# Kernel tuning notes

Measured on AMD Instinct MI355X. Metric: run time of the kernel, lower is better.

Reference implementation:

```python
import jax, jax.numpy as jnp
import numpy as np

NA, NC = 5, 20          # num_anchors, num_classes
EPS, SLOPE = 1e-5, 0.1  # BatchNorm eps, LeakyReLU slope


def _conv(x, w, pad):
    return jax.lax.conv_general_dilated(
        x, w, (1, 1), [(pad, pad), (pad, pad)],
        dimension_numbers=("NCHW", "OIHW", "NCHW"))


def _cbl(x, w, g, b, m, v, pad):
    # Conv2dBatchLeaky: conv (no bias) + eval-mode BN + LeakyReLU(0.1)
    x = _conv(x, w, pad)
    scale = (g * jax.lax.rsqrt(v + EPS))[None, :, None, None]
    shift = (b - m * g * jax.lax.rsqrt(v + EPS))[None, :, None, None]
    x = x * scale + shift
    return jnp.where(x > 0, x, SLOPE * x)


def _reorg(x, s=2):
    # faithful lightnet Reorg: out channels = s*s*C, spatial halved
    B, C, H, W = x.shape
    x = x.reshape(B, C, H // s, s, W // s, s)
    x = x.transpose(0, 1, 2, 4, 3, 5)                 # B,C,H/s,W/s,s,s
    x = x.reshape(B, C, (H // s) * (W // s), s * s)
    x = x.transpose(0, 1, 3, 2)                        # B,C,s*s,HW/s^2
    x = x.reshape(B, C, s * s, H // s, W // s)
    x = x.transpose(0, 2, 1, 3, 4)                     # B,s*s,C,H/s,W/s
    return x.reshape(B, s * s * C, H // s, W // s)


def setup_inputs() -> dict:
    key = jax.random.key(0)
    ks = jax.random.split(key, 16)
    B = 16
    return {
        "feat0": jax.random.normal(ks[0], (B, 1024, 19, 19), jnp.float32),
        "feat1": jax.random.normal(ks[1], (B, 512, 38, 38), jnp.float32),
        "w1": jax.random.normal(ks[2], (64, 512, 1, 1), jnp.float32) * 0.05,
        "g1": jax.random.uniform(ks[3], (64,), jnp.float32, 0.5, 1.5),
        "b1": jax.random.normal(ks[4], (64,), jnp.float32) * 0.05,
        "m1": jax.random.normal(ks[5], (64,), jnp.float32) * 0.05,
        "v1": jax.random.uniform(ks[6], (64,), jnp.float32, 0.5, 1.5),
        "w2": jax.random.normal(ks[7], (1024, 1280, 3, 3), jnp.float32) * 0.01,
        "g2": jax.random.uniform(ks[8], (1024,), jnp.float32, 0.5, 1.5),
        "b2": jax.random.normal(ks[9], (1024,), jnp.float32) * 0.05,
        "m2": jax.random.normal(ks[10], (1024,), jnp.float32) * 0.05,
        "v2": jax.random.uniform(ks[11], (1024,), jnp.float32, 0.5, 1.5),
        "wd": jax.random.normal(ks[12], (30, 1024, 1, 1), jnp.float32) * 0.02,
        "bd": jax.random.normal(ks[13], (30,), jnp.float32) * 0.02,
    }


def reference(feat0, feat1, w1, g1, b1, m1, v1, w2, g2, b2, m2, v2, wd, bd):
    stage6_reorg = _reorg(_cbl(feat1, w1, g1, b1, m1, v1, pad=0))   # B,256,19,19
    pre = _cbl(jnp.concatenate([stage6_reorg, feat0], axis=1),
               w2, g2, b2, m2, v2, pad=1)                            # B,1024,19,19
    B, C, H, W = pre.shape
    # one-hot reweighting mask: channel c belongs to class (c mod NC)
    rew = (jnp.mod(jnp.arange(C, dtype=jnp.float32), NC)[None, :]
           == jnp.arange(NC, dtype=jnp.float32)[:, None]).astype(pre.dtype)  # NC,C
    tiled = pre[:, None] * rew[None, :, :, None, None]               # B,NC,C,H,W
    pred = _conv(tiled.reshape(B * NC, C, H, W), wd, pad=0) \
        + bd[None, :, None, None]                                    # B*NC,30,H,W
    gp = pred.reshape(B, NC, NA, 6, H, W).transpose(0, 2, 1, 3, 4, 5)  # B,NA,NC,6,H,W
    cls = gp[:, :, :, 5]                                             # B,NA,NC,H,W
    ids = jnp.argmax(cls, axis=2)                                    # B,NA,H,W
    g05 = jnp.take_along_axis(gp[:, :, :, :5],
                              ids[:, :, None, None], axis=2)[:, :, 0]  # B,NA,5,H,W
    final = jnp.concatenate([g05, cls], axis=2)                      # B,NA,25,H,W
    return final.reshape(B, NA * (5 + NC), H, W)
```

## Files before the change

### kernel.cpp

```cpp
#include <hip/hip_runtime.h>
#include <hip/hip_bf16.h>

#define EPSV 1e-5f
#define SLOPEV 0.1f
#define AS1 __attribute__((address_space(1)))
#define AS3 __attribute__((address_space(3)))

typedef __attribute__((ext_vector_type(8))) _Float16 h8;
typedef __attribute__((ext_vector_type(4))) float f32x4;
typedef unsigned int uint32;
typedef unsigned short ushort_t;

#define PLANE       ((size_t)18063360)
#define WSPLIT_OFF  ((size_t)36126720)
#define PRE_OFF     ((size_t)124968960)

#define APREC  28224
#define BB     56448
#define BBUF   24576
#define SMEMSZ 105600

__device__ __forceinline__ void split2_pack(const float* f, uint32* ph, uint32* pm) {
#pragma unroll
  for (int i = 0; i < 4; ++i) {
    float a = f[2 * i], b = f[2 * i + 1];
    _Float16 ha = (_Float16)a, hb = (_Float16)b;
    float ra = (a - (float)ha) * 2048.f;
    float rb = (b - (float)hb) * 2048.f;
    _Float16 ma = (_Float16)ra, mb = (_Float16)rb;
    ph[i] = (uint32)__builtin_bit_cast(ushort_t, ha) | ((uint32)__builtin_bit_cast(ushort_t, hb) << 16);
    pm[i] = (uint32)__builtin_bit_cast(ushort_t, ma) | ((uint32)__builtin_bit_cast(ushort_t, mb) << 16);
  }
}

__global__ __launch_bounds__(256) void k_prep(
    const float* __restrict__ feat1, const float* __restrict__ w1,
    const float* __restrict__ g1, const float* __restrict__ b1,
    const float* __restrict__ m1, const float* __restrict__ v1,
    const float* __restrict__ feat0, const float* __restrict__ w2,
    char* __restrict__ nbase, char* __restrict__ wsp)
{
  __shared__ __attribute__((aligned(16))) float S[8192];
  const int bid = blockIdx.x;
  const int t = threadIdx.x;

  if (bid < 384) {
    const int bx = bid % 6, cq = (bid / 6) % 4, b = bid / 24;
#pragma unroll
    for (int i = 0; i < 8; ++i) {
      int f4 = t + i * 256;
      int j = f4 >> 7, c4 = (f4 & 127) * 4;
      *(float4*)&S[j * 512 + c4] = *(const float4*)&w1[(cq * 16 + j) * 512 + c4];
    }
    __syncthreads();
    const int p = bx * 256 + t;
    const int pp = p < 1444 ? p : 1443;
    const float* xp = feat1 + (size_t)(b * 512) * 1444 + pp;
    float acc[16];
#pragma unroll
    for (int j = 0; j < 16; ++j) acc[j] = 0.f;
#pragma unroll 2
    for (int c4 = 0; c4 < 512; c4 += 4) {
      float x0 = xp[(size_t)(c4 + 0) * 1444];
      float x1 = xp[(size_t)(c4 + 1) * 1444];
      float x2 = xp[(size_t)(c4 + 2) * 1444];
      float x3 = xp[(size_t)(c4 + 3) * 1444];
#pragma unroll
      for (int j = 0; j < 16; ++j) {
        float4 w = *(const float4*)&S[j * 512 + c4];
        acc[j] = fmaf(x0, w.x, acc[j]);
        acc[j] = fmaf(x1, w.y, acc[j]);
        acc[j] = fmaf(x2, w.z, acc[j]);
        acc[j] = fmaf(x3, w.w, acc[j]);
      }
    }
    if (p >= 1444) return;
#pragma unroll
    for (int j = 0; j < 16; ++j) {
      int co = cq * 16 + j;
      float sc = g1[co] / sqrtf(v1[co] + EPSV);
      float sh = b1[co] - m1[co] * sc;
      float v = fmaf(acc[j], sc, sh);
      acc[j] = v > 0.f ? v : SLOPEV * v;
    }
    int y = p / 38, x = p - (p / 38) * 38;
    int q = ((y & 1) << 1) | (x & 1);
    int s = (1 + (y >> 1)) * 21 + 1 + (x >> 1);
    const int sw = (s >> 1) & 3;
    size_t rowb = ((size_t)(b * 441 + s)) * 2560;
    int grp = (q * 64 + cq * 16) >> 5;
    char* d0 = nbase + rowb + grp * 64;
#pragma unroll
    for (int u = 0; u < 2; ++u) {
      int q4 = ((cq & 1) << 1) | u;
      uint32 H[4], M[4];
      split2_pack(&acc[u * 8], H, M);
      int off = (q4 ^ sw) << 4;
      *(uint4*)(d0 + off)         = make_uint4(H[0], H[1], H[2], H[3]);
      *(uint4*)(d0 + PLANE + off) = make_uint4(M[0], M[1], M[2], M[3]);
    }

  } else if (bid < 1984) {
    int gid = (bid - 384) * 256 + t;
    int c16 = gid % 160;
    int r = gid / 160;
    int bp = r % 80;
    int pi = r / 80;
    int s;
    if (bp < 21) s = bp;
    else if (bp < 42) s = 399 + bp;
    else if (bp < 61) s = (bp - 41) * 21;
    else s = (bp - 60) * 21 + 20;
    int plane = pi >> 4, img = pi & 15;
    *(uint4*)(nbase + (size_t)plane * PLANE + ((size_t)(img * 441 + s)) * 2560 + c16 * 16)
        = make_uint4(0u, 0u, 0u, 0u);

  } else if (bid < 4544) {
    const int blk = bid - 1984;
    const int cc = blk >> 6, nt = (blk >> 2) & 15, nj = blk & 3;
    const float* src = w2 + ((size_t)(nt * 64 + nj * 16) * 1280 + cc * 32) * 9;
#pragma unroll
    for (int i = 0; i < 18; ++i) {
      int idx = t + i * 256;
      int col = idx / 288, d = idx - col * 288;
      S[col * 289 + d] = src[(size_t)col * 11520 + d];
    }
    __syncthreads();
#pragma unroll
    for (int it = 0; it < 3; ++it) {
      int u = t + it * 256;
      if (u < 576) {
        int tap = u / 64, kq = (u >> 4) & 3, ln = u & 15;
        float f[8];
#pragma unroll
        for (int c8 = 0; c8 < 8; ++c8) f[c8] = S[ln * 289 + (kq * 8 + c8) * 9 + tap] * 32.f;
        uint32 H[4], M[4];
        split2_pack(f, H, M);
        size_t ob = ((size_t)(cc * 16 + nt) * 9 + tap) * 8192 + nj * 1024
                  + (kq * 16 + ln) * 16;
        *(uint4*)(wsp + ob)        = make_uint4(H[0], H[1], H[2], H[3]);
        *(uint4*)(wsp + ob + 4096) = make_uint4(M[0], M[1], M[2], M[3]);
      }
    }

  } else {
    const int bid4 = bid - 4544;
    const int px = bid4 % 6, cy = (bid4 / 6) % 16, b = bid4 / 96;
    const int p0 = px * 64, c0 = 256 + cy * 64;
#pragma unroll
    for (int j = 0; j < 16; ++j) {
      int c_l = (t >> 6) + j * 4;
      int p_l = t & 63;
      float v = 0.f;
      int pos = p0 + p_l;
      if (pos < 361)
        v = feat0[((size_t)(b * 1024 + (c0 - 256) + c_l)) * 361 + pos];
      S[c_l * 65 + p_l] = v;
    }
    __syncthreads();
#pragma unroll
    for (int jj = 0; jj < 2; ++jj) {
      int p_l = (t >> 3) + jj * 32;
      int cgrp = t & 7;
      int pos = p0 + p_l;
      if (pos < 361) {
        int y = pos / 19, x = pos - (pos / 19) * 19;
        int s = (y + 1) * 21 + x + 1;
        float f[8];
#pragma unroll
        for (int u = 0; u < 8; ++u) f[u] = S[(cgrp * 8 + u) * 65 + p_l];
        uint32 H[4], M[4];
        split2_pack(f, H, M);
        int ch8 = c0 + cgrp * 8;
        int grp = ch8 >> 5, q4 = (ch8 >> 3) & 3;
        size_t byteo = ((size_t)(b * 441 + s)) * 2560 + grp * 64
                     + ((q4 ^ ((s >> 1) & 3)) << 4);
        *(uint4*)(nbase + byteo)         = make_uint4(H[0], H[1], H[2], H[3]);
        *(uint4*)(nbase + PLANE + byteo) = make_uint4(M[0], M[1], M[2], M[3]);
      }
    }
  }
}

#define A_ADDR(IDX_) (nbase + (size_t)((IDX_) / 1764) * PLANE + imgbase \
                      + (size_t)((((IDX_) - ((IDX_) / 1764) * 1764)) >> 2) * 2560 \
                      + (ccn << 1) + ((((IDX_) - ((IDX_) / 1764) * 1764) & 3) << 4))

__global__ __launch_bounds__(512, 2) void k_conv2(
    const char* __restrict__ nbase, const char* __restrict__ wsp,
    const float* __restrict__ g2, const float* __restrict__ b2,
    const float* __restrict__ m2, const float* __restrict__ v2,
    float* __restrict__ pre)
{
  __shared__ __attribute__((aligned(16))) unsigned char smem[SMEMSZ];

  const int bid = blockIdx.x;
  const int ntile = (bid & 7) + 8 * ((bid >> 3) & 1);
  const int img = bid >> 4;
  const int co0 = ntile * 64;

  const int tid = threadIdx.x;
  const int wv = tid >> 6;
  const int lane = tid & 63;
  const int ln = lane & 15;
  const int q = lane >> 4;

  int arow[3];
#pragma unroll
  for (int mi = 0; mi < 3; ++mi) {
    int p = wv * 48 + mi * 16 + ln;
    p = p > 360 ? 360 : p;
    arow[mi] = (p / 19) * 21 + (p - (p / 19) * 19);
  }

  f32x4 acc0[3][4], acc1[3][4];
#pragma unroll
  for (int mi = 0; mi < 3; ++mi)
#pragma unroll
    for (int nj = 0; nj < 4; ++nj) { acc0[mi][nj] = (f32x4)0.f; acc1[mi][nj] = (f32x4)0.f; }

  const size_t imgbase = (size_t)(img * 441) * 2560;
  const size_t wnt = (size_t)ntile * 9 * 8192;

#pragma unroll
  for (int i = 0; i < 7; ++i) {
    int idx = tid + i * 512;
    if (idx < 3528) {
      int pr = idx / 1764;
      int r  = idx - pr * 1764;
      const char* src = nbase + (size_t)pr * PLANE + imgbase
                      + (size_t)(r >> 2) * 2560 + ((r & 3) << 4);
      __builtin_amdgcn_global_load_lds((const AS1 uint32*)src,
          (AS3 uint32*)(smem + idx * 16), 16, 0, 0);
    }
  }
  {
    const char* bs = wsp + wnt;
#pragma unroll
    for (int i = 0; i < 3; ++i) {
      int idx = tid + i * 512;
      __builtin_amdgcn_global_load_lds((const AS1 uint32*)(bs + idx * 16),
          (AS3 uint32*)(smem + BB + idx * 16), 16, 0, 0);
    }
  }

  uint4 ar0, ar1, ar2, ar3, ar4, ar5, ar6;

#pragma unroll 1
  for (int cc = 0; cc < 1280; cc += 32) {
    __syncthreads();

    const int ccn = cc + 32;
    const bool pn = ccn < 1280;
    if (pn) {
      ar0 = *(const uint4*)A_ADDR(tid + 0 * 512);
      ar1 = *(const uint4*)A_ADDR(tid + 1 * 512);
      ar2 = *(const uint4*)A_ADDR(tid + 2 * 512);
      ar3 = *(const uint4*)A_ADDR(tid + 3 * 512);
      ar4 = *(const uint4*)A_ADDR(tid + 4 * 512);
      ar5 = *(const uint4*)A_ADDR(tid + 5 * 512);
      if (tid < 456) {
        int r = tid + 3072 - 1764;
        ar6 = *(const uint4*)(nbase + PLANE + imgbase
                + (size_t)(r >> 2) * 2560 + (ccn << 1) + ((r & 3) << 4));
      }
    }

#pragma unroll
    for (int p = 0; p < 3; ++p) {
      const int P = (cc >> 5) * 3 + p;
      if (P + 1 < 120) {
        const int nc = (P + 1) / 3, ntb = ((P + 1) - nc * 3) * 3;
        const char* bs = wsp + ((size_t)nc * 144 + (size_t)ntb) * 8192 + wnt;
        char* bd = (char*)smem + BB + ((P + 1) & 1) * BBUF;
#pragma unroll
        for (int i = 0; i < 3; ++i) {
          int idx = tid + i * 512;
          __builtin_amdgcn_global_load_lds((const AS1 uint32*)(bs + idx * 16),
              (AS3 uint32*)(bd + idx * 16), 16, 0, 0);
        }
      }

      const unsigned char* bufR = smem + BB + (P & 1) * BBUF;
      __builtin_amdgcn_s_setprio(1);
#pragma unroll
      for (int t3 = 0; t3 < 3; ++t3) {
        const int trow = p * 21 + t3;
        h8 A0[3], A1[3];
#pragma unroll
        for (int mi = 0; mi < 3; ++mi) {
          int srow = arow[mi] + trow;
          int aoff = srow * 64 + ((q ^ ((srow >> 1) & 3)) << 4);
          A0[mi] = *(const h8*)(smem + aoff);
          A1[mi] = *(const h8*)(smem + APREC + aoff);
        }
#pragma unroll
        for (int nj = 0; nj < 4; ++nj) {
          const unsigned char* bp0 = bufR + ((t3 * 2 + 0) * 4 + nj) * 1024 + lane * 16;
          h8 B0 = *(const h8*)(bp0);
          h8 B1 = *(const h8*)(bp0 + 4096);
#pragma unroll
          for (int mi = 0; mi < 3; ++mi) {
            acc0[mi][nj] = __builtin_amdgcn_mfma_f32_16x16x32_f16(A0[mi], B0, acc0[mi][nj], 0, 0, 0);
            acc1[mi][nj] = __builtin_amdgcn_mfma_f32_16x16x32_f16(A0[mi], B1, acc1[mi][nj], 0, 0, 0);
            acc1[mi][nj] = __builtin_amdgcn_mfma_f32_16x16x32_f16(A1[mi], B0, acc1[mi][nj], 0, 0, 0);
          }
        }
      }
      __builtin_amdgcn_s_setprio(0);
      __syncthreads();
    }

    if (pn) {
      *(uint4*)(smem + (tid + 0 * 512) * 16) = ar0;
      *(uint4*)(smem + (tid + 1 * 512) * 16) = ar1;
      *(uint4*)(smem + (tid + 2 * 512) * 16) = ar2;
      *(uint4*)(smem + (tid + 3 * 512) * 16) = ar3;
      *(uint4*)(smem + (tid + 4 * 512) * 16) = ar4;
      *(uint4*)(smem + (tid + 5 * 512) * 16) = ar5;
      if (tid < 456)
        *(uint4*)(smem + (tid + 3072) * 16) = ar6;
    }
  }

#pragma unroll
  for (int nj = 0; nj < 4; ++nj) {
    int co = co0 + nj * 16 + ln;
    float sc = g2[co] / sqrtf(v2[co] + EPSV) * 0.03125f;
    float sh = b2[co] - m2[co] * (sc * 32.f);
    float* op = pre + ((size_t)(img * 1024 + co)) * 361;
#pragma unroll
    for (int mi = 0; mi < 3; ++mi) {
#pragma unroll
      for (int r = 0; r < 4; ++r) {
        int p = wv * 48 + mi * 16 + q * 4 + r;
        if (p < 361) {
          float t = fmaf(acc1[mi][nj][r], 4.8828125e-4f, acc0[mi][nj][r]);
          float v = fmaf(t, sc, sh);
          v = v > 0.f ? v : SLOPEV * v;
          op[p] = v;
        }
      }
    }
  }
}

__global__ __launch_bounds__(384) void k_pred(
    const float* __restrict__ pre, const float* __restrict__ wd,
    const float* __restrict__ bd, float* __restrict__ pred)
{
  __shared__ float W[30 * 52];
  const int k = blockIdx.x;
  const int b = blockIdx.y;
  const int t = threadIdx.x;
  const int nj = (1023 - k) / 20 + 1;

  for (int u = t; u < 30 * 52; u += 384) {
    int o = u / 52, j = u - o * 52;
    W[u] = (j < nj) ? wd[o * 1024 + k + 20 * j] : 0.f;
  }
  __syncthreads();
  if (t >= 361) return;

  const float* xb = pre + (size_t)b * 1024 * 361 + t;
  float acc[30];
#pragma unroll
  for (int o = 0; o < 30; ++o) acc[o] = 0.f;
  for (int j = 0; j < nj; ++j) {
    float x = xb[(size_t)(k + 20 * j) * 361];
#pragma unroll
    for (int o = 0; o < 30; ++o) acc[o] = fmaf(W[o * 52 + j], x, acc[o]);
  }
  float* ob = pred + ((size_t)(b * 20 + k) * 30) * 361 + t;
#pragma unroll
  for (int o = 0; o < 30; ++o) ob[(size_t)o * 361] = acc[o] + bd[o];
}

__global__ __launch_bounds__(64) void k_sel(
    const float* __restrict__ pred, float* __restrict__ out)
{
  const int ph = blockIdx.x, a = blockIdx.y, b = blockIdx.z;
  const int p = ph * 64 + threadIdx.x;
  const bool act = p < 361;
  const int pp = act ? p : 360;
  const float* pb = pred + (size_t)b * 20 * 30 * 361 + pp;

  float best = -3.4e38f; int bidx = 0;
  float cls[20];
#pragma unroll
  for (int kk = 0; kk < 20; ++kk) {
    float s = pb[(size_t)(kk * 30 + a * 6 + 5) * 361];
    cls[kk] = s;
    if (s > best) { best = s; bidx = kk; }
  }
  if (!act) return;
#pragma unroll
  for (int kk = 0; kk < 20; ++kk)
    out[((size_t)(b * 125 + a * 25 + 5 + kk)) * 361 + p] = cls[kk];
#pragma unroll
  for (int j = 0; j < 5; ++j)
    out[((size_t)(b * 125 + a * 25 + j)) * 361 + p]
        = pb[(size_t)(bidx * 30 + a * 6 + j) * 361];
}

extern "C" void kernel_launch(void* const* d_in, const int* in_sizes, int n_in,
                              void* d_out, int out_size, void* d_ws, size_t ws_size,
                              hipStream_t stream)
{
  const float* feat0 = (const float*)d_in[0];
  const float* feat1 = (const float*)d_in[1];
  const float* w1    = (const float*)d_in[2];
  const float* g1    = (const float*)d_in[3];
  const float* b1    = (const float*)d_in[4];
  const float* m1    = (const float*)d_in[5];
  const float* v1    = (const float*)d_in[6];
  const float* w2    = (const float*)d_in[7];
  const float* g2    = (const float*)d_in[8];
  const float* b2    = (const float*)d_in[9];
  const float* m2    = (const float*)d_in[10];
  const float* v2    = (const float*)d_in[11];
  const float* wd    = (const float*)d_in[12];
  const float* bd    = (const float*)d_in[13];
  float* out = (float*)d_out;

  char*  nbase = (char*)d_ws;
  char*  wsp   = (char*)d_ws + WSPLIT_OFF;
  float* pre   = (float*)((char*)d_ws + PRE_OFF);
  float* pred  = (float*)((char*)d_ws + WSPLIT_OFF);

  k_prep<<<dim3(6080), 256, 0, stream>>>(feat1, w1, g1, b1, m1, v1, feat0, w2, nbase, wsp);
  k_conv2<<<dim3(256), 512, 0, stream>>>(nbase, wsp, g2, b2, m2, v2, pre);
  k_pred<<<dim3(20, 16), 384, 0, stream>>>(pre, wd, bd, pred);
  k_sel<<<dim3(6, 5, 16), 64, 0, stream>>>(pred, out);
}
```

Measured before the change: 450.5 us.

## Halve conv2 channel tile, double grid, read mantissa plane from global

The 3x3 conv kernel now gives each block 32 output channels instead of 64 and launches 512 blocks with a launch bound of four blocks per SM. LDS drops to about half: only the high-precision activation plane and a smaller double-buffered weight tile stay in shared memory. The residual (mantissa) plane is read straight from global memory inside the MFMA loop. The register-staged prefetch of the next activation chunk is replaced by a direct global-to-LDS load at the top of each channel chunk. The goal is more resident waves and fewer idle CUs. In exchange, activations are fetched twice overall, the activation load is no longer overlapped with compute, the global reads in the inner loop add latency, and the tighter register budget may cause spills.

```diff
diff --git a/kernel.cpp b/kernel.cpp
--- a/kernel.cpp
+++ b/kernel.cpp
@@ -16,9 +16,8 @@
 #define PRE_OFF     ((size_t)124968960)
 
 #define APREC  28224
-#define BB     56448
-#define BBUF   24576
-#define SMEMSZ 105600
+#define BBUF   12288
+#define SMEMSZ 52800
 
 __device__ __forceinline__ void split2_pack(const float* f, uint32* ph, uint32* pm) {
 #pragma unroll
@@ -182,11 +181,7 @@
   }
 }
 
-#define A_ADDR(IDX_) (nbase + (size_t)((IDX_) / 1764) * PLANE + imgbase \
-                      + (size_t)((((IDX_) - ((IDX_) / 1764) * 1764)) >> 2) * 2560 \
-                      + (ccn << 1) + ((((IDX_) - ((IDX_) / 1764) * 1764) & 3) << 4))
-
-__global__ __launch_bounds__(512, 2) void k_conv2(
+__global__ __launch_bounds__(512, 4) void k_conv2(
     const char* __restrict__ nbase, const char* __restrict__ wsp,
     const float* __restrict__ g2, const float* __restrict__ b2,
     const float* __restrict__ m2, const float* __restrict__ v2,
@@ -195,9 +190,10 @@
   __shared__ __attribute__((aligned(16))) unsigned char smem[SMEMSZ];
 
   const int bid = blockIdx.x;
-  const int ntile = (bid & 7) + 8 * ((bid >> 3) & 1);
-  const int img = bid >> 4;
-  const int co0 = ntile * 64;
+  const int n2 = bid & 31;
+  const int img = bid >> 5;
+  const int co0 = n2 * 32;
+  const int njb = (n2 & 1) * 2;
 
   const int tid = threadIdx.x;
   const int wv = tid >> 6;
@@ -213,58 +209,46 @@
     arow[mi] = (p / 19) * 21 + (p - (p / 19) * 19);
   }
 
-  f32x4 acc0[3][4], acc1[3][4];
+  f32x4 acc0[3][2], acc1[3][2];
 #pragma unroll
   for (int mi = 0; mi < 3; ++mi)
 #pragma unroll
-    for (int nj = 0; nj < 4; ++nj) { acc0[mi][nj] = (f32x4)0.f; acc1[mi][nj] = (f32x4)0.f; }
+    for (int nj = 0; nj < 2; ++nj) { acc0[mi][nj] = (f32x4)0.f; acc1[mi][nj] = (f32x4)0.f; }
 
   const size_t imgbase = (size_t)(img * 441) * 2560;
-  const size_t wnt = (size_t)ntile * 9 * 8192;
-
-#pragma unroll
-  for (int i = 0; i < 7; ++i) {
-    int idx = tid + i * 512;
-    if (idx < 3528) {
-      int pr = idx / 1764;
-      int r  = idx - pr * 1764;
-      const char* src = nbase + (size_t)pr * PLANE + imgbase
-                      + (size_t)(r >> 2) * 2560 + ((r & 3) << 4);
-      __builtin_amdgcn_global_load_lds((const AS1 uint32*)src,
-          (AS3 uint32*)(smem + idx * 16), 16, 0, 0);
-    }
-  }
+  const size_t wnt = (size_t)(n2 >> 1) * 9 * 8192;
+  const char* mplane = nbase + PLANE + imgbase;
+
   {
     const char* bs = wsp + wnt;
 #pragma unroll
-    for (int i = 0; i < 3; ++i) {
+    for (int i = 0; i < 2; ++i) {
       int idx = tid + i * 512;
-      __builtin_amdgcn_global_load_lds((const AS1 uint32*)(bs + idx * 16),
-          (AS3 uint32*)(smem + BB + idx * 16), 16, 0, 0);
-    }
-  }
-
-  uint4 ar0, ar1, ar2, ar3, ar4, ar5, ar6;
+      if (idx < 768) {
+        int t3s = idx >> 8, r = idx & 255;
+        int prec = r >> 7, njx = (r >> 6) & 1, w = r & 63;
+        __builtin_amdgcn_global_load_lds(
+            (const AS1 uint32*)(bs + t3s * 8192 + prec * 4096 + (njb + njx) * 1024 + w * 16),
+            (AS3 uint32*)(smem + APREC + idx * 16), 16, 0, 0);
+      }
+    }
+  }
 
 #pragma unroll 1
   for (int cc = 0; cc < 1280; cc += 32) {
+#pragma unroll
+    for (int i = 0; i < 4; ++i) {
+      int idx = tid + i * 512;
+      if (idx < 1764) {
+        const char* src = nbase + imgbase + (size_t)(idx >> 2) * 2560
+                        + (cc << 1) + ((idx & 3) << 4);
+        __builtin_amdgcn_global_load_lds((const AS1 uint32*)src,
+            (AS3 uint32*)(smem + idx * 16), 16, 0, 0);
+      }
+    }
     __syncthreads();
 
-    const int ccn = cc + 32;
-    const bool pn = ccn < 1280;
-    if (pn) {
-      ar0 = *(const uint4*)A_ADDR(tid + 0 * 512);
-      ar1 = *(const uint4*)A_ADDR(tid + 1 * 512);
-      ar2 = *(const uint4*)A_ADDR(tid + 2 * 512);
-      ar3 = *(const uint4*)A_ADDR(tid + 3 * 512);
-      ar4 = *(const uint4*)A_ADDR(tid + 4 * 512);
-      ar5 = *(const uint4*)A_ADDR(tid + 5 * 512);
-      if (tid < 456) {
-        int r = tid + 3072 - 1764;
-        ar6 = *(const uint4*)(nbase + PLANE + imgbase
-                + (size_t)(r >> 2) * 2560 + (ccn << 1) + ((r & 3) << 4));
-      }
-    }
+    const char* mrow = mplane + (cc << 1);
 
 #pragma unroll
     for (int p = 0; p < 3; ++p) {
@@ -272,16 +256,21 @@
       if (P + 1 < 120) {
         const int nc = (P + 1) / 3, ntb = ((P + 1) - nc * 3) * 3;
         const char* bs = wsp + ((size_t)nc * 144 + (size_t)ntb) * 8192 + wnt;
-        char* bd = (char*)smem + BB + ((P + 1) & 1) * BBUF;
-#pragma unroll
-        for (int i = 0; i < 3; ++i) {
+        char* bd = (char*)smem + APREC + ((P + 1) & 1) * BBUF;
+#pragma unroll
+        for (int i = 0; i < 2; ++i) {
           int idx = tid + i * 512;
-          __builtin_amdgcn_global_load_lds((const AS1 uint32*)(bs + idx * 16),
-              (AS3 uint32*)(bd + idx * 16), 16, 0, 0);
+          if (idx < 768) {
+            int t3s = idx >> 8, r = idx & 255;
+            int prec = r >> 7, njx = (r >> 6) & 1, w = r & 63;
+            __builtin_amdgcn_global_load_lds(
+                (const AS1 uint32*)(bs + t3s * 8192 + prec * 4096 + (njb + njx) * 1024 + w * 16),
+                (AS3 uint32*)(bd + idx * 16), 16, 0, 0);
+          }
         }
       }
 
-      const unsigned char* bufR = smem + BB + (P & 1) * BBUF;
+      const unsigned char* bufR = smem + APREC + (P & 1) * BBUF;
       __builtin_amdgcn_s_setprio(1);
 #pragma unroll
       for (int t3 = 0; t3 < 3; ++t3) {
@@ -290,15 +279,15 @@
 #pragma unroll
         for (int mi = 0; mi < 3; ++mi) {
           int srow = arow[mi] + trow;
-          int aoff = srow * 64 + ((q ^ ((srow >> 1) & 3)) << 4);
-          A0[mi] = *(const h8*)(smem + aoff);
-          A1[mi] = *(const h8*)(smem + APREC + aoff);
+          int swo = (q ^ ((srow >> 1) & 3)) << 4;
+          A0[mi] = *(const h8*)(smem + srow * 64 + swo);
+          A1[mi] = *(const h8*)(mrow + (size_t)srow * 2560 + swo);
         }
 #pragma unroll
-        for (int nj = 0; nj < 4; ++nj) {
-          const unsigned char* bp0 = bufR + ((t3 * 2 + 0) * 4 + nj) * 1024 + lane * 16;
+        for (int nj = 0; nj < 2; ++nj) {
+          const unsigned char* bp0 = bufR + t3 * 4096 + nj * 1024 + lane * 16;
           h8 B0 = *(const h8*)(bp0);
-          h8 B1 = *(const h8*)(bp0 + 4096);
+          h8 B1 = *(const h8*)(bp0 + 2048);
 #pragma unroll
           for (int mi = 0; mi < 3; ++mi) {
             acc0[mi][nj] = __builtin_amdgcn_mfma_f32_16x16x32_f16(A0[mi], B0, acc0[mi][nj], 0, 0, 0);
@@ -310,21 +299,10 @@
       __builtin_amdgcn_s_setprio(0);
       __syncthreads();
     }
-
-    if (pn) {
-      *(uint4*)(smem + (tid + 0 * 512) * 16) = ar0;
-      *(uint4*)(smem + (tid + 1 * 512) * 16) = ar1;
-      *(uint4*)(smem + (tid + 2 * 512) * 16) = ar2;
-      *(uint4*)(smem + (tid + 3 * 512) * 16) = ar3;
-      *(uint4*)(smem + (tid + 4 * 512) * 16) = ar4;
-      *(uint4*)(smem + (tid + 5 * 512) * 16) = ar5;
-      if (tid < 456)
-        *(uint4*)(smem + (tid + 3072) * 16) = ar6;
-    }
-  }
-
-#pragma unroll
-  for (int nj = 0; nj < 4; ++nj) {
+  }
+
+#pragma unroll
+  for (int nj = 0; nj < 2; ++nj) {
     int co = co0 + nj * 16 + ln;
     float sc = g2[co] / sqrtf(v2[co] + EPSV) * 0.03125f;
     float sh = b2[co] - m2[co] * (sc * 32.f);
@@ -429,7 +407,7 @@
   float* pred  = (float*)((char*)d_ws + WSPLIT_OFF);
 
   k_prep<<<dim3(6080), 256, 0, stream>>>(feat1, w1, g1, b1, m1, v1, feat0, w2, nbase, wsp);
-  k_conv2<<<dim3(256), 512, 0, stream>>>(nbase, wsp, g2, b2, m2, v2, pre);
+  k_conv2<<<dim3(512), 512, 0, stream>>>(nbase, wsp, g2, b2, m2, v2, pre);
   k_pred<<<dim3(20, 16), 384, 0, stream>>>(pre, wd, bd, pred);
   k_sel<<<dim3(6, 5, 16), 64, 0, stream>>>(pred, out);
 }
```

After: 959.4 us. +113.0%, slower.

## Double-buffer conv2 activation tile in LDS via async global_load_lds

Applied to the files above, without the earlier changes.

The next activation channel chunk used to be prefetched into registers (seven uint4 per thread) and stored to LDS after compute. It is now loaded asynchronously straight into a second LDS buffer, spread across the three inner p-steps, and the buffers ping-pong. The aim is to remove register pressure and the serial LDS store phase so loads overlap with MFMA work. LDS use rises from about 103KB to 158KB per block, which may lower occupancy below the two blocks per CU requested by launch bounds.

```diff
diff --git a/kernel.cpp b/kernel.cpp
--- a/kernel.cpp
+++ b/kernel.cpp
@@ -16,9 +16,10 @@
 #define PRE_OFF     ((size_t)124968960)
 
 #define APREC  28224
-#define BB     56448
+#define ABUF   56448
+#define BOFF   112896
 #define BBUF   24576
-#define SMEMSZ 105600
+#define SMEMSZ 162048
 
 __device__ __forceinline__ void split2_pack(const float* f, uint32* ph, uint32* pm) {
 #pragma unroll
@@ -182,10 +183,6 @@
   }
 }
 
-#define A_ADDR(IDX_) (nbase + (size_t)((IDX_) / 1764) * PLANE + imgbase \
-                      + (size_t)((((IDX_) - ((IDX_) / 1764) * 1764)) >> 2) * 2560 \
-                      + (ccn << 1) + ((((IDX_) - ((IDX_) / 1764) * 1764) & 3) << 4))
-
 __global__ __launch_bounds__(512, 2) void k_conv2(
     const char* __restrict__ nbase, const char* __restrict__ wsp,
     const float* __restrict__ g2, const float* __restrict__ b2,
@@ -240,31 +237,18 @@
     for (int i = 0; i < 3; ++i) {
       int idx = tid + i * 512;
       __builtin_amdgcn_global_load_lds((const AS1 uint32*)(bs + idx * 16),
-          (AS3 uint32*)(smem + BB + idx * 16), 16, 0, 0);
-    }
-  }
-
-  uint4 ar0, ar1, ar2, ar3, ar4, ar5, ar6;
+          (AS3 uint32*)(smem + BOFF + idx * 16), 16, 0, 0);
+    }
+  }
+  __syncthreads();
 
 #pragma unroll 1
   for (int cc = 0; cc < 1280; cc += 32) {
-    __syncthreads();
-
+    const int cur = (cc >> 5) & 1;
+    const unsigned char* aCur = smem + cur * ABUF;
+    char* aNext = (char*)smem + (cur ^ 1) * ABUF;
     const int ccn = cc + 32;
     const bool pn = ccn < 1280;
-    if (pn) {
-      ar0 = *(const uint4*)A_ADDR(tid + 0 * 512);
-      ar1 = *(const uint4*)A_ADDR(tid + 1 * 512);
-      ar2 = *(const uint4*)A_ADDR(tid + 2 * 512);
-      ar3 = *(const uint4*)A_ADDR(tid + 3 * 512);
-      ar4 = *(const uint4*)A_ADDR(tid + 4 * 512);
-      ar5 = *(const uint4*)A_ADDR(tid + 5 * 512);
-      if (tid < 456) {
-        int r = tid + 3072 - 1764;
-        ar6 = *(const uint4*)(nbase + PLANE + imgbase
-                + (size_t)(r >> 2) * 2560 + (ccn << 1) + ((r & 3) << 4));
-      }
-    }
 
 #pragma unroll
     for (int p = 0; p < 3; ++p) {
@@ -272,7 +256,7 @@
       if (P + 1 < 120) {
         const int nc = (P + 1) / 3, ntb = ((P + 1) - nc * 3) * 3;
         const char* bs = wsp + ((size_t)nc * 144 + (size_t)ntb) * 8192 + wnt;
-        char* bd = (char*)smem + BB + ((P + 1) & 1) * BBUF;
+        char* bd = (char*)smem + BOFF + ((P + 1) & 1) * BBUF;
 #pragma unroll
         for (int i = 0; i < 3; ++i) {
           int idx = tid + i * 512;
@@ -280,8 +264,22 @@
               (AS3 uint32*)(bd + idx * 16), 16, 0, 0);
         }
       }
-
-      const unsigned char* bufR = smem + BB + (P & 1) * BBUF;
+      if (pn) {
+#pragma unroll
+        for (int i = 0; i < 3; ++i) {
+          int idx = p * 1176 + i * 512 + tid;
+          if (idx < (p + 1) * 1176) {
+            int pr = idx / 1764;
+            int r  = idx - pr * 1764;
+            const char* src = nbase + (size_t)pr * PLANE + imgbase
+                            + (size_t)(r >> 2) * 2560 + (ccn << 1) + ((r & 3) << 4);
+            __builtin_amdgcn_global_load_lds((const AS1 uint32*)src,
+                (AS3 uint32*)(aNext + idx * 16), 16, 0, 0);
+          }
+        }
+      }
+
+      const unsigned char* bufR = smem + BOFF + (P & 1) * BBUF;
       __builtin_amdgcn_s_setprio(1);
 #pragma unroll
       for (int t3 = 0; t3 < 3; ++t3) {
@@ -291,12 +289,12 @@
         for (int mi = 0; mi < 3; ++mi) {
           int srow = arow[mi] + trow;
           int aoff = srow * 64 + ((q ^ ((srow >> 1) & 3)) << 4);
-          A0[mi] = *(const h8*)(smem + aoff);
-          A1[mi] = *(const h8*)(smem + APREC + aoff);
+          A0[mi] = *(const h8*)(aCur + aoff);
+          A1[mi] = *(const h8*)(aCur + APREC + aoff);
         }
 #pragma unroll
         for (int nj = 0; nj < 4; ++nj) {
-          const unsigned char* bp0 = bufR + ((t3 * 2 + 0) * 4 + nj) * 1024 + lane * 16;
+          const unsigned char* bp0 = bufR + t3 * 8192 + nj * 1024 + lane * 16;
           h8 B0 = *(const h8*)(bp0);
           h8 B1 = *(const h8*)(bp0 + 4096);
 #pragma unroll
@@ -309,17 +307,6 @@
       }
       __builtin_amdgcn_s_setprio(0);
       __syncthreads();
-    }
-
-    if (pn) {
-      *(uint4*)(smem + (tid + 0 * 512) * 16) = ar0;
-      *(uint4*)(smem + (tid + 1 * 512) * 16) = ar1;
-      *(uint4*)(smem + (tid + 2 * 512) * 16) = ar2;
-      *(uint4*)(smem + (tid + 3 * 512) * 16) = ar3;
-      *(uint4*)(smem + (tid + 4 * 512) * 16) = ar4;
-      *(uint4*)(smem + (tid + 5 * 512) * 16) = ar5;
-      if (tid < 456)
-        *(uint4*)(smem + (tid + 3072) * 16) = ar6;
     }
   }
 
```

New measurement: 440.9 us. 1.02x faster.
